# Performance work log

Hardware: AMD Instinct MI355X
Metric: run time of the kernel (lower is better)

Reference implementation:

```python
import jax, jax.numpy as jnp
import numpy as np
import math

# Static problem sizes (match input_specs)
B, TQ, SQ, TK, SK = 1, 8, 256, 32, 1024
DM, NH = 1024, 8
HD = DM // NH            # 128; mrope_section sums to HD//2
MROPE = [16, 24, 24]
ROPE_BASE = 10000.0


def _build_indices():
    """Reproduce create_idx_cube + slow/fast index selection (all static)."""
    T_max = max(TQ, TK)
    H_max = int(math.sqrt(max(SQ, SK)))
    cube = np.stack(np.meshgrid(np.arange(T_max), np.arange(H_max), np.arange(H_max), indexing='ij'), axis=-1)  # (T,H,W,3)
    # slow (query) indices
    t_idx = np.linspace(0, T_max - 1, TQ).astype(int)
    slow = cube[t_idx]
    if SQ < SK:
        h_q = int(math.sqrt(SQ))
        hi = np.linspace(0, H_max, 2 * h_q + 1).astype(int)[1:-1][::2]
        slow = slow[:, hi][:, :, hi]
    # fast (key) indices
    h_k = int(math.sqrt(SK))
    hf = np.linspace(0, H_max, 2 * h_k + 1).astype(int)[1:-1][::2]
    fast = cube[:, hf][:, :, hf]
    return slow.reshape(-1, 3).T, fast.reshape(-1, 3).T, max(T_max, H_max)


_slow_np, _fast_np, _SEQ = _build_indices()
SLOW_POS = jnp.asarray(_slow_np)   # (3, TQ*SQ) int
FAST_POS = jnp.asarray(_fast_np)   # (3, TK*SK) int

# Standard rotary tables: cos/sin of shape (seq_len, HD)
_inv = 1.0 / (ROPE_BASE ** (np.arange(0, HD, 2, dtype=np.float32) / HD))
_freqs = np.outer(np.arange(_SEQ, dtype=np.float32), _inv)
_emb = np.concatenate([_freqs, _freqs], axis=-1)
COS = jnp.asarray(np.cos(_emb), dtype=jnp.float32)
SIN = jnp.asarray(np.sin(_emb), dtype=jnp.float32)

# per-channel axis (t/h/w) selector, equivalent to the split/concat with i%3
AXIS_MAP = jnp.asarray(np.concatenate([np.full(m, i % 3) for i, m in enumerate(MROPE * 2)]))  # (HD,)


def rotate_half(x):
    return jnp.concatenate([-x[..., HD // 2:], x[..., :HD // 2]], axis=-1)


def apply_mrope(x, pos):
    # x: (B, NH, N, HD); pos: (3, N)
    cos_g = jnp.take_along_axis(COS[pos], AXIS_MAP[None, None, :], axis=0)[0]  # (N, HD)
    sin_g = jnp.take_along_axis(SIN[pos], AXIS_MAP[None, None, :], axis=0)[0]
    return x * cos_g[None, None] + rotate_half(x) * sin_g[None, None]


def setup_inputs() -> dict:
    key = jax.random.key(0)
    ks = jax.random.split(key, 9)
    s = 0.02
    return {
        'q': jax.random.normal(ks[0], (B, TQ, SQ, DM), jnp.float32),
        'k': jax.random.normal(ks[1], (B, TK, SK, DM), jnp.float32),
        'v': jax.random.normal(ks[2], (B, TK, SK, DM), jnp.float32),
        'Wq': jax.random.normal(ks[3], (DM, DM), jnp.float32) * s,
        'bq': jnp.zeros((DM,), jnp.float32),
        'Wk': jax.random.normal(ks[4], (DM, DM), jnp.float32) * s,
        'bk': jnp.zeros((DM,), jnp.float32),
        'Wv': jax.random.normal(ks[5], (DM, DM), jnp.float32) * s,
        'bv': jnp.zeros((DM,), jnp.float32),
    }


def reference(q, k, v, Wq, bq, Wk, bk, Wv, bv):
    # QKV projections -> (B, NH, N, HD)
    qh = (q.reshape(B, TQ * SQ, DM) @ Wq + bq).reshape(B, TQ * SQ, NH, HD).transpose(0, 2, 1, 3)
    kh = (k.reshape(B, TK * SK, DM) @ Wk + bk).reshape(B, TK * SK, NH, HD).transpose(0, 2, 1, 3)
    vh = (v.reshape(B, TK * SK, DM) @ Wv + bv).reshape(B, TK * SK, NH, HD).transpose(0, 2, 1, 3)
    # multimodal 3D RoPE on q (slow frames) and k (fast frames)
    qh = apply_mrope(qh, SLOW_POS)
    kh = apply_mrope(kh, FAST_POS)
    # group time: each query frame attends to its r = TK//TQ aligned kv frames
    r = TK // TQ
    qg = qh.reshape(NH, TQ, SQ, HD).transpose(1, 0, 2, 3)          # (TQ, NH, SQ, HD)
    kg = kh.reshape(NH, TQ, r * SK, HD).transpose(1, 0, 2, 3)      # (TQ, NH, r*SK, HD)
    vg = vh.reshape(NH, TQ, r * SK, HD).transpose(1, 0, 2, 3)
    scores = jnp.einsum('thqd,thkd->thqk', qg, kg) / math.sqrt(HD)
    attn = jax.nn.softmax(scores, axis=-1)
    out = jnp.einsum('thqk,thkd->thqd', attn, vg)                  # (TQ, NH, SQ, HD)
    return out.transpose(0, 2, 1, 3).reshape(B, TQ, SQ, DM)
```

## Files before the change

kernel.cpp:

```cpp
#include <hip/hip_runtime.h>

typedef __bf16 bf16;
typedef __bf16 bf16x8 __attribute__((ext_vector_type(8)));
typedef float  f32x4  __attribute__((ext_vector_type(4)));

#define MFMA16(a, b, c) __builtin_amdgcn_mfma_f32_16x16x32_bf16((a), (b), (c), 0, 0, 0)

#define GLOAD_LDS16(gptr, lptr)                                              \
    __builtin_amdgcn_global_load_lds(                                        \
        (const __attribute__((address_space(1))) unsigned int*)(gptr),       \
        (__attribute__((address_space(3))) unsigned int*)(lptr), 16, 0, 0)

constexpr int kDM = 1024;
constexpr int kNTOK = 32768;

static __device__ inline f32x4 zero4() { f32x4 z = {0.f, 0.f, 0.f, 0.f}; return z; }

__global__ __launch_bounds__(256) void transpose_all(
    const float* __restrict__ Wq, const float* __restrict__ Wk,
    const float* __restrict__ Wv, bf16* __restrict__ Wqt,
    bf16* __restrict__ Wkt, bf16* __restrict__ Wvt)
{
    __shared__ bf16 T[64][68];
    const float* W = (blockIdx.z == 0) ? Wq : (blockIdx.z == 1) ? Wk : Wv;
    bf16* Wt       = (blockIdx.z == 0) ? Wqt : (blockIdx.z == 1) ? Wkt : Wvt;
    const int tid = threadIdx.x;
    const int n0 = blockIdx.x * 64, k0 = blockIdx.y * 64;
    #pragma unroll
    for (int i = 0; i < 4; i++) {
        const int kk = (tid >> 4) + i * 16, nn4 = (tid & 15) * 4;
        float4 v = *(const float4*)&W[(size_t)(k0 + kk) * kDM + n0 + nn4];
        T[nn4 + 0][kk] = (bf16)v.x; T[nn4 + 1][kk] = (bf16)v.y;
        T[nn4 + 2][kk] = (bf16)v.z; T[nn4 + 3][kk] = (bf16)v.w;
    }
    __syncthreads();
    #pragma unroll
    for (int i = 0; i < 4; i++) {
        const int nn = (tid >> 4) + i * 16, kc = (tid & 15) * 4;
        *(ushort4*)&Wt[(size_t)(n0 + nn) * kDM + k0 + kc] = *(const ushort4*)&T[nn][kc];
    }
}

template <int MODE>
__global__ __launch_bounds__(256) void gemm_fused(
    const float* __restrict__ X, const bf16* __restrict__ Wt,
    const float* __restrict__ bias, bf16* __restrict__ out, int mtiles_per_xcd)
{
    __shared__ char smem[49152];
    float* Af = (float*)smem;
    bf16*  Bb = (bf16*)(smem + 32768);
    bf16*  Y  = (bf16*)smem;

    const int b    = blockIdx.x;
    const int xcd  = b & 7;
    const int s    = b >> 3;
    const int m0   = (xcd * mtiles_per_xcd + (s >> 3)) * 128;
    const int n0   = (s & 7) * 128;
    const int tid  = threadIdx.x;
    const int wave = tid >> 6;
    const int lane = tid & 63;
    const int quad = lane >> 4, l16 = lane & 15;
    const int mb   = (wave & 1) * 64, nb = (wave >> 1) * 64;

    f32x4 acc[4][4];
    #pragma unroll
    for (int i = 0; i < 4; i++)
        #pragma unroll
        for (int j = 0; j < 4; j++) acc[i][j] = zero4();

    for (int k0 = 0; k0 < kDM; k0 += 64) {
        __syncthreads();
        #pragma unroll
        for (int i = 0; i < 8; i++) {
            const int c = wave * 8 + i;
            const int row = c * 4 + (lane >> 4);
            const int sl  = lane & 15;
            const int src = ((((sl >> 1) ^ (row & 7)) << 1) | (sl & 1)) * 4;
            GLOAD_LDS16(&X[(size_t)(m0 + row) * kDM + k0 + src], &Af[c * 256]);
        }
        #pragma unroll
        for (int i = 0; i < 4; i++) {
            const int c = wave * 4 + i;
            const int row = c * 8 + (lane >> 3);
            GLOAD_LDS16(&Wt[(size_t)(n0 + row) * kDM + k0 + (((lane & 7) ^ (row & 7)) * 8)],
                        &Bb[c * 512]);
        }
        __syncthreads();
        #pragma unroll
        for (int ks = 0; ks < 2; ks++) {
            bf16x8 a[4], bfr[4];
            #pragma unroll
            for (int i = 0; i < 4; i++) {
                const int m = mb + i * 16 + l16;
                const int G = (ks * 4 + quad) ^ (l16 & 7);
                const float* p = &Af[m * 64 + G * 8];
                f32x4 u0 = *(const f32x4*)p;
                f32x4 u1 = *(const f32x4*)(p + 4);
                #pragma unroll
                for (int e = 0; e < 4; e++) { a[i][e] = (bf16)u0[e]; a[i][4 + e] = (bf16)u1[e]; }
            }
            #pragma unroll
            for (int j = 0; j < 4; j++) {
                const int n = nb + j * 16 + l16;
                bfr[j] = *(const bf16x8*)&Bb[n * 64 + (((ks * 4 + quad) ^ (l16 & 7)) * 8)];
            }
            #pragma unroll
            for (int i = 0; i < 4; i++)
                #pragma unroll
                for (int j = 0; j < 4; j++)
                    acc[i][j] = MFMA16(a[i], bfr[j], acc[i][j]);
        }
    }

    __syncthreads();

    if (MODE == 3) {
        #pragma unroll
        for (int j = 0; j < 4; j++) {
            const int n = nb + j * 16 + l16;
            const float bv = bias[n0 + n];
            #pragma unroll
            for (int i = 0; i < 4; i++) {
                const int m = mb + i * 16 + quad * 4;
                bf16 tmp[4];
                #pragma unroll
                for (int r = 0; r < 4; r++) tmp[r] = (bf16)(acc[i][j][r] + bv);
                *(ushort4*)&Y[n * 136 + m] = *(const ushort4*)tmp;
            }
        }
        __syncthreads();
        const int row = tid >> 1, seg = (tid & 1) * 64;
        #pragma unroll
        for (int kk = 0; kk < 8; kk++)
            *(uint4*)&out[(size_t)(n0 + row) * kNTOK + m0 + seg + kk * 8] =
                *(const uint4*)&Y[row * 136 + seg + kk * 8];
    } else {
        if (wave >= 2) {
            #pragma unroll
            for (int j = 0; j < 4; j++) {
                const int dcol = 64 + j * 16 + l16;
                const float bv = bias[n0 + dcol];
                #pragma unroll
                for (int i = 0; i < 4; i++)
                    #pragma unroll
                    for (int r = 0; r < 4; r++)
                        Y[(mb + i * 16 + quad * 4 + r) * 136 + dcol] =
                            (bf16)(acc[i][j][r] + bv);
            }
        }
        __syncthreads();
        if (wave < 2) {
            #pragma unroll
            for (int j = 0; j < 4; j++) {
                const int d = j * 16 + l16;
                const float bv = bias[n0 + d];
                const float invf = exp2f((float)d * -0.20762050593045951f);
                #pragma unroll
                for (int i = 0; i < 4; i++) {
                    #pragma unroll
                    for (int r = 0; r < 4; r++) {
                        const int mloc = mb + i * 16 + quad * 4 + r;
                        const int tok = m0 + mloc;
                        int pt, ph, pw;
                        if (MODE == 2) { pt = tok >> 10; ph = (tok >> 5) & 31; pw = tok & 31; }
                        else { int tq = tok >> 8; pt = (31 * tq) / 7;
                               ph = 2 * ((tok >> 4) & 15) + 1; pw = 2 * (tok & 15) + 1; }
                        const int p = (d < 16) ? pt : ((d < 40) ? ph : pw);
                        float sn, cs;
                        __sincosf((float)p * invf, &sn, &cs);
                        const float x1 = acc[i][j][r] + bv;
                        const float x2 = (float)Y[mloc * 136 + 64 + d];
                        Y[mloc * 136 + d]      = (bf16)(x1 * cs - x2 * sn);
                        Y[mloc * 136 + 64 + d] = (bf16)(x2 * cs + x1 * sn);
                    }
                }
            }
        }
        __syncthreads();
        const int row = tid >> 1, seg = (tid & 1) * 64;
        #pragma unroll
        for (int kk = 0; kk < 8; kk++)
            *(uint4*)&out[(size_t)(m0 + row) * kDM + n0 + seg + kk * 8] =
                *(const uint4*)&Y[row * 136 + seg + kk * 8];
    }
}

__global__ __launch_bounds__(256) void attn_kernel(
    const bf16* __restrict__ qh, const bf16* __restrict__ kh,
    const bf16* __restrict__ vt, float* __restrict__ Opart, float* __restrict__ ml)
{
    __shared__ bf16 Ks[64 * 128];
    __shared__ bf16 Vs[128 * 64];
    __shared__ bf16 Ps[4][16][64];

    const int tid  = threadIdx.x;
    const int z    = blockIdx.x, h = blockIdx.y, qb = blockIdx.z;
    const int t    = z >> 2, sp = z & 3;
    const int wave = tid >> 6;
    const int lane = tid & 63;
    const int quad = lane >> 4, l16 = lane & 15;

    const int qrow = qb * 64 + wave * 16 + l16;
    const size_t qbase = ((size_t)(t * 256 + qrow)) * kDM + h * 128;
    bf16x8 aq[4];
    #pragma unroll
    for (int kb = 0; kb < 4; kb++)
        aq[kb] = *(const bf16x8*)&qh[qbase + kb * 32 + quad * 8];

    bf16x8 ones;
    #pragma unroll
    for (int e = 0; e < 8; e++) ones[e] = (bf16)1.0f;

    f32x4 o[9];
    #pragma unroll
    for (int j = 0; j < 9; j++) o[j] = zero4();
    float m_run[4];
    #pragma unroll
    for (int r = 0; r < 4; r++) m_run[r] = -1e30f;
    const float scale = 0.08838834764831845f;

    const int r16 = lane >> 4, j16 = lane & 15;
    const int r8  = lane >> 3, j8  = lane & 7;

    for (int kt = 0; kt < 16; kt++) {
        const int kbase = t * 4096 + sp * 1024 + kt * 64;
        __syncthreads();
        #pragma unroll
        for (int i = 0; i < 4; i++) {
            const int c = wave * 4 + i;
            const int krow = c * 4 + r16;
            GLOAD_LDS16(&kh[(size_t)(kbase + krow) * kDM + h * 128 + ((j16 ^ (krow & 15)) * 8)],
                        &Ks[c * 512]);
        }
        #pragma unroll
        for (int i = 0; i < 4; i++) {
            const int c = wave * 4 + i;
            GLOAD_LDS16(&vt[(size_t)(h * 128 + c * 8 + r8) * kNTOK + kbase + ((j8 ^ r8) * 8)],
                        &Vs[c * 512]);
        }
        __syncthreads();

        f32x4 s[4];
        #pragma unroll
        for (int c = 0; c < 4; c++) s[c] = zero4();
        #pragma unroll
        for (int kb = 0; kb < 4; kb++) {
            #pragma unroll
            for (int c = 0; c < 4; c++) {
                bf16x8 b = *(const bf16x8*)&Ks[(c * 16 + l16) * 128 + (((kb * 4 + quad) ^ l16) * 8)];
                s[c] = MFMA16(aq[kb], b, s[c]);
            }
        }

        float alpha[4];
        #pragma unroll
        for (int r = 0; r < 4; r++) {
            float sv[4];
            #pragma unroll
            for (int c = 0; c < 4; c++) sv[c] = s[c][r] * scale;
            float mx = fmaxf(fmaxf(sv[0], sv[1]), fmaxf(sv[2], sv[3]));
            #pragma unroll
            for (int off = 1; off < 16; off <<= 1) mx = fmaxf(mx, __shfl_xor(mx, off));
            const float mn = fmaxf(m_run[r], mx);
            alpha[r] = __expf(m_run[r] - mn);
            m_run[r] = mn;
            const int q7 = quad * 4 + r;
            #pragma unroll
            for (int c = 0; c < 4; c++) {
                const int col = (c * 16 + l16) ^ ((q7 & 7) * 8);
                Ps[wave][q7][col] = (bf16)__expf(sv[c] - mn);
            }
        }
        #pragma unroll
        for (int j = 0; j < 9; j++)
            #pragma unroll
            for (int r = 0; r < 4; r++) o[j][r] *= alpha[r];
        #pragma unroll
        for (int ks = 0; ks < 2; ks++) {
            bf16x8 pa = *(const bf16x8*)&Ps[wave][l16][((ks * 4 + quad) ^ (l16 & 7)) * 8];
            #pragma unroll
            for (int j = 0; j < 8; j++) {
                bf16x8 bv = *(const bf16x8*)&Vs[(j * 16 + l16) * 64 + (((ks * 4 + quad) ^ (l16 & 7)) * 8)];
                o[j] = MFMA16(pa, bv, o[j]);
            }
            o[8] = MFMA16(pa, ones, o[8]);
        }
    }

    #pragma unroll
    for (int r = 0; r < 4; r++) {
        const int srow = qb * 64 + wave * 16 + quad * 4 + r;
        const size_t pr = ((size_t)(z * 8 + h)) * 256 + srow;
        #pragma unroll
        for (int j = 0; j < 8; j++)
            Opart[pr * 128 + j * 16 + l16] = o[j][r];
        if (l16 == 0) { ml[pr * 2] = m_run[r]; ml[pr * 2 + 1] = o[8][r]; }
    }
}

__global__ __launch_bounds__(256) void combine_kernel(
    const float* __restrict__ Opart, const float* __restrict__ ml,
    float* __restrict__ out)
{
    const int tid = threadIdx.x;
    const int rid = blockIdx.x * 2 + (tid >> 7);
    const int d   = tid & 127;
    const int t = rid >> 11, h = (rid >> 8) & 7, srow = rid & 255;

    float mv[4], lv[4];
    #pragma unroll
    for (int sp = 0; sp < 4; sp++) {
        const size_t pr = ((size_t)((t * 4 + sp) * 8 + h)) * 256 + srow;
        float2 p = *(const float2*)&ml[pr * 2];
        mv[sp] = p.x; lv[sp] = p.y;
    }
    const float ms = fmaxf(fmaxf(mv[0], mv[1]), fmaxf(mv[2], mv[3]));
    float lsum = 0.f, acc = 0.f;
    #pragma unroll
    for (int sp = 0; sp < 4; sp++) {
        const size_t pr = ((size_t)((t * 4 + sp) * 8 + h)) * 256 + srow;
        const float w = __expf(mv[sp] - ms);
        lsum += lv[sp] * w;
        acc  += Opart[pr * 128 + d] * w;
    }
    out[((size_t)(t * 256 + srow)) * kDM + h * 128 + d] = acc / lsum;
}

extern "C" void kernel_launch(void* const* d_in, const int* in_sizes, int n_in,
                              void* d_out, int out_size, void* d_ws, size_t ws_size,
                              hipStream_t stream)
{
    const float* q  = (const float*)d_in[0];
    const float* k  = (const float*)d_in[1];
    const float* v  = (const float*)d_in[2];
    const float* Wq = (const float*)d_in[3];
    const float* bq = (const float*)d_in[4];
    const float* Wk = (const float*)d_in[5];
    const float* bk = (const float*)d_in[6];
    const float* Wv = (const float*)d_in[7];
    const float* bv = (const float*)d_in[8];
    float* out = (float*)d_out;

    bf16* qh  = (bf16*)d_ws;
    bf16* kh  = qh + (size_t)2048 * 1024;
    bf16* vt  = kh + (size_t)32768 * 1024;
    bf16* Wqt = vt + (size_t)32768 * 1024;
    bf16* Wkt = Wqt + (size_t)1024 * 1024;
    bf16* Wvt = Wkt + (size_t)1024 * 1024;
    float* Opart = (float*)(Wvt + (size_t)1024 * 1024);
    float* ml    = Opart + (size_t)32 * 8 * 256 * 128;

    transpose_all<<<dim3(16, 16, 3), 256, 0, stream>>>(Wq, Wk, Wv, Wqt, Wkt, Wvt);
    gemm_fused<1><<<128,  256, 0, stream>>>(q, Wqt, bq, qh, 2);
    gemm_fused<2><<<2048, 256, 0, stream>>>(k, Wkt, bk, kh, 32);
    gemm_fused<3><<<2048, 256, 0, stream>>>(v, Wvt, bv, vt, 32);
    attn_kernel<<<dim3(32, 8, 4), 256, 0, stream>>>(qh, kh, vt, Opart, ml);
    combine_kernel<<<8192, 256, 0, stream>>>(Opart, ml, out);
}
```

Baseline: 638.1 us.

## Enlarge projection GEMM tiles to 256x256 with double-buffered bf16 LDS staging

Restructures the QKV projection GEMM to use 512-thread blocks that each compute a 256x256 output tile, in place of 128x128. The K loop is now double-buffered: fp32 activations for the next step are loaded into registers, converted to bf16 and written to the alternate LDS buffer, while weights stream in via direct-to-LDS loads during the current MFMA step. The RoPE and transposed-V epilogues are split into two 128-column halves so they fit the LDS layout. The goal is to cut redundant global reads and per-step barrier stalls, at the cost of much more LDS (128 KB), more accumulator registers, and only 32 blocks for the Q projection.

```diff
diff --git a/kernel.cpp b/kernel.cpp
--- a/kernel.cpp
+++ b/kernel.cpp
@@ -42,146 +42,197 @@
 }
 
 template <int MODE>
-__global__ __launch_bounds__(256) void gemm_fused(
+__global__ __launch_bounds__(512, 2) void gemm_fused(
     const float* __restrict__ X, const bf16* __restrict__ Wt,
     const float* __restrict__ bias, bf16* __restrict__ out, int mtiles_per_xcd)
 {
-    __shared__ char smem[49152];
-    float* Af = (float*)smem;
-    bf16*  Bb = (bf16*)(smem + 32768);
-    bf16*  Y  = (bf16*)smem;
+    __shared__ char smem[131072];
 
     const int b    = blockIdx.x;
     const int xcd  = b & 7;
     const int s    = b >> 3;
-    const int m0   = (xcd * mtiles_per_xcd + (s >> 3)) * 128;
-    const int n0   = (s & 7) * 128;
+    const int m0   = (xcd * mtiles_per_xcd + (s >> 2)) * 256;
+    const int n0   = (s & 3) * 256;
     const int tid  = threadIdx.x;
     const int wave = tid >> 6;
     const int lane = tid & 63;
     const int quad = lane >> 4, l16 = lane & 15;
-    const int mb   = (wave & 1) * 64, nb = (wave >> 1) * 64;
-
-    f32x4 acc[4][4];
-    #pragma unroll
-    for (int i = 0; i < 4; i++)
+    const int wr   = wave >> 2;
+    const int wc   = wave & 3;
+
+    const int arow  = tid >> 3;
+    const int as8   = tid & 7;
+    const int awoff = (as8 ^ (arow & 7)) * 8;
+    const float* xbase = X + (size_t)(m0 + arow) * kDM + as8 * 8;
+    const int bc0 = wave * 4;
+
+    f32x4 acc[8][4];
+    #pragma unroll
+    for (int i = 0; i < 8; i++)
         #pragma unroll
         for (int j = 0; j < 4; j++) acc[i][j] = zero4();
 
-    for (int k0 = 0; k0 < kDM; k0 += 64) {
-        __syncthreads();
-        #pragma unroll
-        for (int i = 0; i < 8; i++) {
-            const int c = wave * 8 + i;
-            const int row = c * 4 + (lane >> 4);
-            const int sl  = lane & 15;
-            const int src = ((((sl >> 1) ^ (row & 7)) << 1) | (sl & 1)) * 4;
-            GLOAD_LDS16(&X[(size_t)(m0 + row) * kDM + k0 + src], &Af[c * 256]);
-        }
+    {
         #pragma unroll
         for (int i = 0; i < 4; i++) {
-            const int c = wave * 4 + i;
-            const int row = c * 8 + (lane >> 3);
-            GLOAD_LDS16(&Wt[(size_t)(n0 + row) * kDM + k0 + (((lane & 7) ^ (row & 7)) * 8)],
-                        &Bb[c * 512]);
-        }
-        __syncthreads();
-        #pragma unroll
-        for (int ks = 0; ks < 2; ks++) {
-            bf16x8 a[4], bfr[4];
+            const int row = (bc0 + i) * 8 + (lane >> 3);
+            GLOAD_LDS16(&Wt[(size_t)(n0 + row) * kDM + (((lane & 7) ^ (row & 7)) * 8)],
+                        (bf16*)(smem + 65536) + (bc0 + i) * 512);
+        }
+        #pragma unroll
+        for (int p = 0; p < 4; p++) {
+            const float* src = xbase + (size_t)p * 64 * kDM;
+            float4 u0 = *(const float4*)src;
+            float4 u1 = *(const float4*)(src + 4);
+            bf16x8 w;
+            #pragma unroll
+            for (int e = 0; e < 4; e++) { w[e] = (bf16)u0[e]; w[4 + e] = (bf16)u1[e]; }
+            *(bf16x8*)&((bf16*)smem)[(p * 64 + arow) * 64 + awoff] = w;
+        }
+        asm volatile("s_waitcnt lgkmcnt(0)" ::: "memory");
+        asm volatile("s_waitcnt vmcnt(0)" ::: "memory");
+        __builtin_amdgcn_s_barrier();
+    }
+
+    for (int t = 0; t < 16; ++t) {
+        const int bt = t & 1;
+        bf16* Ac = (bf16*)(smem + bt * 32768);
+        bf16* An = (bf16*)(smem + (bt ^ 1) * 32768);
+        bf16* Bc = (bf16*)(smem + 65536 + bt * 32768);
+        bf16* Bn = (bf16*)(smem + 65536 + (bt ^ 1) * 32768);
+
+        float4 av[8];
+        if (t < 15) {
+            const int k1 = (t + 1) * 64;
+            #pragma unroll
+            for (int p = 0; p < 4; p++) {
+                const float* src = xbase + (size_t)p * 64 * kDM + k1;
+                av[p * 2]     = *(const float4*)src;
+                av[p * 2 + 1] = *(const float4*)(src + 4);
+            }
             #pragma unroll
             for (int i = 0; i < 4; i++) {
-                const int m = mb + i * 16 + l16;
-                const int G = (ks * 4 + quad) ^ (l16 & 7);
-                const float* p = &Af[m * 64 + G * 8];
-                f32x4 u0 = *(const f32x4*)p;
-                f32x4 u1 = *(const f32x4*)(p + 4);
-                #pragma unroll
-                for (int e = 0; e < 4; e++) { a[i][e] = (bf16)u0[e]; a[i][4 + e] = (bf16)u1[e]; }
-            }
-            #pragma unroll
-            for (int j = 0; j < 4; j++) {
-                const int n = nb + j * 16 + l16;
-                bfr[j] = *(const bf16x8*)&Bb[n * 64 + (((ks * 4 + quad) ^ (l16 & 7)) * 8)];
-            }
-            #pragma unroll
-            for (int i = 0; i < 4; i++)
+                const int row = (bc0 + i) * 8 + (lane >> 3);
+                GLOAD_LDS16(&Wt[(size_t)(n0 + row) * kDM + k1 + (((lane & 7) ^ (row & 7)) * 8)],
+                            Bn + (bc0 + i) * 512);
+            }
+        }
+        __builtin_amdgcn_sched_barrier(0);
+
+        #pragma unroll
+        for (int ks = 0; ks < 2; ++ks) {
+            bf16x8 a[8], bq[4];
+            const int G = ks * 4 + quad;
+            #pragma unroll
+            for (int i = 0; i < 8; i++)
+                a[i] = *(const bf16x8*)&Ac[(wr * 128 + i * 16 + l16) * 64 + ((G ^ (l16 & 7)) * 8)];
+            #pragma unroll
+            for (int j = 0; j < 4; j++)
+                bq[j] = *(const bf16x8*)&Bc[(wc * 64 + j * 16 + l16) * 64 + ((G ^ (l16 & 7)) * 8)];
+            #pragma unroll
+            for (int i = 0; i < 8; i++)
                 #pragma unroll
                 for (int j = 0; j < 4; j++)
-                    acc[i][j] = MFMA16(a[i], bfr[j], acc[i][j]);
-        }
-    }
-
-    __syncthreads();
+                    acc[i][j] = MFMA16(a[i], bq[j], acc[i][j]);
+        }
+
+        if (t < 15) {
+            #pragma unroll
+            for (int p = 0; p < 4; p++) {
+                bf16x8 w;
+                #pragma unroll
+                for (int e = 0; e < 4; e++) {
+                    w[e]     = (bf16)av[p * 2][e];
+                    w[4 + e] = (bf16)av[p * 2 + 1][e];
+                }
+                *(bf16x8*)&An[(p * 64 + arow) * 64 + awoff] = w;
+            }
+        }
+        asm volatile("s_waitcnt lgkmcnt(0)" ::: "memory");
+        asm volatile("s_waitcnt vmcnt(0)" ::: "memory");
+        __builtin_amdgcn_s_barrier();
+    }
 
     if (MODE == 3) {
-        #pragma unroll
-        for (int j = 0; j < 4; j++) {
-            const int n = nb + j * 16 + l16;
-            const float bv = bias[n0 + n];
-            #pragma unroll
-            for (int i = 0; i < 4; i++) {
-                const int m = mb + i * 16 + quad * 4;
-                bf16 tmp[4];
+        bf16* Y3 = (bf16*)smem;
+        #pragma unroll
+        for (int h = 0; h < 2; h++) {
+            if ((wc >> 1) == h) {
                 #pragma unroll
-                for (int r = 0; r < 4; r++) tmp[r] = (bf16)(acc[i][j][r] + bv);
-                *(ushort4*)&Y[n * 136 + m] = *(const ushort4*)tmp;
-            }
-        }
-        __syncthreads();
-        const int row = tid >> 1, seg = (tid & 1) * 64;
-        #pragma unroll
-        for (int kk = 0; kk < 8; kk++)
-            *(uint4*)&out[(size_t)(n0 + row) * kNTOK + m0 + seg + kk * 8] =
-                *(const uint4*)&Y[row * 136 + seg + kk * 8];
-    } else {
-        if (wave >= 2) {
-            #pragma unroll
-            for (int j = 0; j < 4; j++) {
-                const int dcol = 64 + j * 16 + l16;
-                const float bv = bias[n0 + dcol];
-                #pragma unroll
-                for (int i = 0; i < 4; i++)
+                for (int j = 0; j < 4; j++) {
+                    const int nl = (wc & 1) * 64 + j * 16 + l16;
+                    const float bv = bias[n0 + wc * 64 + j * 16 + l16];
                     #pragma unroll
-                    for (int r = 0; r < 4; r++)
-                        Y[(mb + i * 16 + quad * 4 + r) * 136 + dcol] =
-                            (bf16)(acc[i][j][r] + bv);
-            }
-        }
-        __syncthreads();
-        if (wave < 2) {
-            #pragma unroll
-            for (int j = 0; j < 4; j++) {
-                const int d = j * 16 + l16;
-                const float bv = bias[n0 + d];
-                const float invf = exp2f((float)d * -0.20762050593045951f);
-                #pragma unroll
-                for (int i = 0; i < 4; i++) {
-                    #pragma unroll
-                    for (int r = 0; r < 4; r++) {
-                        const int mloc = mb + i * 16 + quad * 4 + r;
-                        const int tok = m0 + mloc;
-                        int pt, ph, pw;
-                        if (MODE == 2) { pt = tok >> 10; ph = (tok >> 5) & 31; pw = tok & 31; }
-                        else { int tq = tok >> 8; pt = (31 * tq) / 7;
-                               ph = 2 * ((tok >> 4) & 15) + 1; pw = 2 * (tok & 15) + 1; }
-                        const int p = (d < 16) ? pt : ((d < 40) ? ph : pw);
-                        float sn, cs;
-                        __sincosf((float)p * invf, &sn, &cs);
-                        const float x1 = acc[i][j][r] + bv;
-                        const float x2 = (float)Y[mloc * 136 + 64 + d];
-                        Y[mloc * 136 + d]      = (bf16)(x1 * cs - x2 * sn);
-                        Y[mloc * 136 + 64 + d] = (bf16)(x2 * cs + x1 * sn);
+                    for (int i = 0; i < 8; i++) {
+                        bf16 tmp[4];
+                        #pragma unroll
+                        for (int r = 0; r < 4; r++) tmp[r] = (bf16)(acc[i][j][r] + bv);
+                        *(ushort4*)&Y3[nl * 264 + wr * 128 + i * 16 + quad * 4] =
+                            *(const ushort4*)tmp;
                     }
                 }
             }
-        }
-        __syncthreads();
-        const int row = tid >> 1, seg = (tid & 1) * 64;
-        #pragma unroll
-        for (int kk = 0; kk < 8; kk++)
-            *(uint4*)&out[(size_t)(m0 + row) * kDM + n0 + seg + kk * 8] =
-                *(const uint4*)&Y[row * 136 + seg + kk * 8];
+            __syncthreads();
+            const int nl = tid >> 5, m8 = (tid & 31) * 8;
+            #pragma unroll
+            for (int kk = 0; kk < 8; kk++)
+                *(uint4*)&out[(size_t)(n0 + h * 128 + nl + kk * 16) * kNTOK + m0 + m8] =
+                    *(const uint4*)&Y3[(nl + kk * 16) * 264 + m8];
+            __syncthreads();
+        }
+    } else {
+        bf16* Y = (bf16*)smem;
+        #pragma unroll
+        for (int h = 0; h < 2; h++) {
+            if ((wc >> 1) == h && (wc & 1)) {
+                #pragma unroll
+                for (int j = 0; j < 4; j++) {
+                    const int dj = j * 16 + l16;
+                    const float bv = bias[n0 + wc * 64 + j * 16 + l16];
+                    #pragma unroll
+                    for (int i = 0; i < 8; i++)
+                        #pragma unroll
+                        for (int r = 0; r < 4; r++)
+                            Y[(wr * 128 + i * 16 + quad * 4 + r) * 136 + 64 + dj] =
+                                (bf16)(acc[i][j][r] + bv);
+                }
+            }
+            __syncthreads();
+            if ((wc >> 1) == h && !(wc & 1)) {
+                #pragma unroll
+                for (int j = 0; j < 4; j++) {
+                    const int d = j * 16 + l16;
+                    const float bv = bias[n0 + wc * 64 + j * 16 + l16];
+                    const float invf = exp2f((float)d * -0.20762050593045951f);
+                    #pragma unroll
+                    for (int i = 0; i < 8; i++) {
+                        #pragma unroll
+                        for (int r = 0; r < 4; r++) {
+                            const int mloc = wr * 128 + i * 16 + quad * 4 + r;
+                            const int tok = m0 + mloc;
+                            int pt, ph, pw;
+                            if (MODE == 2) { pt = tok >> 10; ph = (tok >> 5) & 31; pw = tok & 31; }
+                            else { int tq = tok >> 8; pt = (31 * tq) / 7;
+                                   ph = 2 * ((tok >> 4) & 15) + 1; pw = 2 * (tok & 15) + 1; }
+                            const int p = (d < 16) ? pt : ((d < 40) ? ph : pw);
+                            float sn, cs;
+                            __sincosf((float)p * invf, &sn, &cs);
+                            const float x1 = acc[i][j][r] + bv;
+                            const float x2 = (float)Y[mloc * 136 + 64 + d];
+                            Y[mloc * 136 + d]      = (bf16)(x1 * cs - x2 * sn);
+                            Y[mloc * 136 + 64 + d] = (bf16)(x2 * cs + x1 * sn);
+                        }
+                    }
+                }
+            }
+            __syncthreads();
+            const int rrow = tid >> 1, seg = (tid & 1) * 64;
+            #pragma unroll
+            for (int kk = 0; kk < 8; kk++)
+                *(uint4*)&out[(size_t)(m0 + rrow) * kDM + n0 + h * 128 + seg + kk * 8] =
+                    *(const uint4*)&Y[rrow * 136 + seg + kk * 8];
+            __syncthreads();
+        }
     }
 }
 
@@ -351,9 +402,9 @@
     float* ml    = Opart + (size_t)32 * 8 * 256 * 128;
 
     transpose_all<<<dim3(16, 16, 3), 256, 0, stream>>>(Wq, Wk, Wv, Wqt, Wkt, Wvt);
-    gemm_fused<1><<<128,  256, 0, stream>>>(q, Wqt, bq, qh, 2);
-    gemm_fused<2><<<2048, 256, 0, stream>>>(k, Wkt, bk, kh, 32);
-    gemm_fused<3><<<2048, 256, 0, stream>>>(v, Wvt, bv, vt, 32);
+    gemm_fused<1><<<32,  512, 0, stream>>>(q, Wqt, bq, qh, 1);
+    gemm_fused<2><<<512, 512, 0, stream>>>(k, Wkt, bk, kh, 16);
+    gemm_fused<3><<<512, 512, 0, stream>>>(v, Wvt, bv, vt, 16);
     attn_kernel<<<dim3(32, 8, 4), 256, 0, stream>>>(qh, kh, vt, Opart, ml);
     combine_kernel<<<8192, 256, 0, stream>>>(Opart, ml, out);
 }
```

New measurement: 650.5 us. About the same (+1.9%).

## Pre-convert GEMM inputs to bf16 and raise wave priority around attention MFMAs

Applied to the files above, without the earlier changes.

Adds a separate conversion pass that writes the q/k/v activations as bf16 into a workspace buffer. The projection GEMMs can then load bf16 tiles straight into LDS, which halves LDS use and drops the per-fragment fp32-to-bf16 conversion in the inner loop. The cost is an extra full read and write of each input tensor, roughly 128MB fp32 read plus 64MB bf16 written for k and v, so total HBM traffic goes up. Separately, s_setprio is raised around the MFMA blocks in the attention kernel to favour matrix issue.

```diff
diff --git a/kernel.cpp b/kernel.cpp
--- a/kernel.cpp
+++ b/kernel.cpp
@@ -15,6 +15,21 @@
 constexpr int kNTOK = 32768;
 
 static __device__ inline f32x4 zero4() { f32x4 z = {0.f, 0.f, 0.f, 0.f}; return z; }
+
+__global__ __launch_bounds__(256) void cvt_bf16(
+    const float* __restrict__ src, bf16* __restrict__ dst, int n8)
+{
+    int idx = blockIdx.x * 256 + threadIdx.x;
+    const int stride = gridDim.x * 256;
+    for (; idx < n8; idx += stride) {
+        const float4 u0 = *(const float4*)(src + (size_t)idx * 8);
+        const float4 u1 = *(const float4*)(src + (size_t)idx * 8 + 4);
+        bf16x8 w;
+        w[0] = (bf16)u0.x; w[1] = (bf16)u0.y; w[2] = (bf16)u0.z; w[3] = (bf16)u0.w;
+        w[4] = (bf16)u1.x; w[5] = (bf16)u1.y; w[6] = (bf16)u1.z; w[7] = (bf16)u1.w;
+        *(bf16x8*)&dst[(size_t)idx * 8] = w;
+    }
+}
 
 __global__ __launch_bounds__(256) void transpose_all(
     const float* __restrict__ Wq, const float* __restrict__ Wk,
@@ -43,13 +58,13 @@
 
 template <int MODE>
 __global__ __launch_bounds__(256) void gemm_fused(
-    const float* __restrict__ X, const bf16* __restrict__ Wt,
+    const bf16* __restrict__ Xb, const bf16* __restrict__ Wt,
     const float* __restrict__ bias, bf16* __restrict__ out, int mtiles_per_xcd)
 {
-    __shared__ char smem[49152];
-    float* Af = (float*)smem;
-    bf16*  Bb = (bf16*)(smem + 32768);
-    bf16*  Y  = (bf16*)smem;
+    __shared__ char smem[34816];
+    bf16* Ab = (bf16*)smem;
+    bf16* Bb = (bf16*)(smem + 16384);
+    bf16* Y  = (bf16*)smem;
 
     const int b    = blockIdx.x;
     const int xcd  = b & 7;
@@ -61,6 +76,7 @@
     const int lane = tid & 63;
     const int quad = lane >> 4, l16 = lane & 15;
     const int mb   = (wave & 1) * 64, nb = (wave >> 1) * 64;
+    const int r8   = lane >> 3, j8 = lane & 7;
 
     f32x4 acc[4][4];
     #pragma unroll
@@ -70,40 +86,31 @@
 
     for (int k0 = 0; k0 < kDM; k0 += 64) {
         __syncthreads();
-        #pragma unroll
-        for (int i = 0; i < 8; i++) {
-            const int c = wave * 8 + i;
-            const int row = c * 4 + (lane >> 4);
-            const int sl  = lane & 15;
-            const int src = ((((sl >> 1) ^ (row & 7)) << 1) | (sl & 1)) * 4;
-            GLOAD_LDS16(&X[(size_t)(m0 + row) * kDM + k0 + src], &Af[c * 256]);
-        }
         #pragma unroll
         for (int i = 0; i < 4; i++) {
             const int c = wave * 4 + i;
-            const int row = c * 8 + (lane >> 3);
-            GLOAD_LDS16(&Wt[(size_t)(n0 + row) * kDM + k0 + (((lane & 7) ^ (row & 7)) * 8)],
+            const int row = c * 8 + r8;
+            GLOAD_LDS16(&Xb[(size_t)(m0 + row) * kDM + k0 + ((j8 ^ (row & 7)) * 8)],
+                        &Ab[c * 512]);
+        }
+        #pragma unroll
+        for (int i = 0; i < 4; i++) {
+            const int c = wave * 4 + i;
+            const int row = c * 8 + r8;
+            GLOAD_LDS16(&Wt[(size_t)(n0 + row) * kDM + k0 + ((j8 ^ (row & 7)) * 8)],
                         &Bb[c * 512]);
         }
         __syncthreads();
         #pragma unroll
         for (int ks = 0; ks < 2; ks++) {
+            const int G = ks * 4 + quad;
             bf16x8 a[4], bfr[4];
             #pragma unroll
-            for (int i = 0; i < 4; i++) {
-                const int m = mb + i * 16 + l16;
-                const int G = (ks * 4 + quad) ^ (l16 & 7);
-                const float* p = &Af[m * 64 + G * 8];
-                f32x4 u0 = *(const f32x4*)p;
-                f32x4 u1 = *(const f32x4*)(p + 4);
-                #pragma unroll
-                for (int e = 0; e < 4; e++) { a[i][e] = (bf16)u0[e]; a[i][4 + e] = (bf16)u1[e]; }
-            }
-            #pragma unroll
-            for (int j = 0; j < 4; j++) {
-                const int n = nb + j * 16 + l16;
-                bfr[j] = *(const bf16x8*)&Bb[n * 64 + (((ks * 4 + quad) ^ (l16 & 7)) * 8)];
-            }
+            for (int i = 0; i < 4; i++)
+                a[i] = *(const bf16x8*)&Ab[(mb + i * 16 + l16) * 64 + ((G ^ (l16 & 7)) * 8)];
+            #pragma unroll
+            for (int j = 0; j < 4; j++)
+                bfr[j] = *(const bf16x8*)&Bb[(nb + j * 16 + l16) * 64 + ((G ^ (l16 & 7)) * 8)];
             #pragma unroll
             for (int i = 0; i < 4; i++)
                 #pragma unroll
@@ -243,6 +250,7 @@
         f32x4 s[4];
         #pragma unroll
         for (int c = 0; c < 4; c++) s[c] = zero4();
+        __builtin_amdgcn_s_setprio(1);
         #pragma unroll
         for (int kb = 0; kb < 4; kb++) {
             #pragma unroll
@@ -251,6 +259,7 @@
                 s[c] = MFMA16(aq[kb], b, s[c]);
             }
         }
+        __builtin_amdgcn_s_setprio(0);
 
         float alpha[4];
         #pragma unroll
@@ -275,6 +284,7 @@
         for (int j = 0; j < 9; j++)
             #pragma unroll
             for (int r = 0; r < 4; r++) o[j][r] *= alpha[r];
+        __builtin_amdgcn_s_setprio(1);
         #pragma unroll
         for (int ks = 0; ks < 2; ks++) {
             bf16x8 pa = *(const bf16x8*)&Ps[wave][l16][((ks * 4 + quad) ^ (l16 & 7)) * 8];
@@ -285,6 +295,7 @@
             }
             o[8] = MFMA16(pa, ones, o[8]);
         }
+        __builtin_amdgcn_s_setprio(0);
     }
 
     #pragma unroll
@@ -349,11 +360,19 @@
     bf16* Wvt = Wkt + (size_t)1024 * 1024;
     float* Opart = (float*)(Wvt + (size_t)1024 * 1024);
     float* ml    = Opart + (size_t)32 * 8 * 256 * 128;
+    bf16* Xb     = (bf16*)(ml + (size_t)32 * 8 * 256 * 2);
 
     transpose_all<<<dim3(16, 16, 3), 256, 0, stream>>>(Wq, Wk, Wv, Wqt, Wkt, Wvt);
-    gemm_fused<1><<<128,  256, 0, stream>>>(q, Wqt, bq, qh, 2);
-    gemm_fused<2><<<2048, 256, 0, stream>>>(k, Wkt, bk, kh, 32);
-    gemm_fused<3><<<2048, 256, 0, stream>>>(v, Wvt, bv, vt, 32);
+
+    cvt_bf16<<<512, 256, 0, stream>>>(q, Xb, 2048 * 1024 / 8);
+    gemm_fused<1><<<128,  256, 0, stream>>>(Xb, Wqt, bq, qh, 2);
+
+    cvt_bf16<<<2048, 256, 0, stream>>>(k, Xb, 32768 * 1024 / 8);
+    gemm_fused<2><<<2048, 256, 0, stream>>>(Xb, Wkt, bk, kh, 32);
+
+    cvt_bf16<<<2048, 256, 0, stream>>>(v, Xb, 32768 * 1024 / 8);
+    gemm_fused<3><<<2048, 256, 0, stream>>>(Xb, Wvt, bv, vt, 32);
+
     attn_kernel<<<dim3(32, 8, 4), 256, 0, stream>>>(qh, kh, vt, Opart, ml);
     combine_kernel<<<8192, 256, 0, stream>>>(Opart, ml, out);
 }
```

After: 635.3 us. Within noise of the previous version (-0.4%).
